# Kernel optimization log

Hardware: AMD Instinct MI355X
Metric: run time of the kernel (lower is better)

Reference implementation:

```python
import jax, jax.numpy as jnp
import numpy as np

E = 64          # num_expert
DIN = 512       # d_input
DOUT = 512      # d_output
T = 131072      # total routed tokens (sum of fwd_expert_count)


def setup_inputs() -> dict:
    key = jax.random.key(0)
    k1, k2, k3 = jax.random.split(key, 3)
    inp = jax.random.normal(k1, (T, DIN), dtype=jnp.float32)
    # FMoELinear params: weight [E, d_out, d_in], bias [E, d_out]
    weight = jax.random.normal(k2, (E, DOUT, DIN), dtype=jnp.float32) * (1.0 / np.sqrt(DIN))
    bias = jax.random.normal(k3, (E, DOUT), dtype=jnp.float32) * 0.01
    # Irregular per-expert token counts summing exactly to T (host-side int64,
    # as in fastmoe where fwd_expert_count lives on CPU and drives dispatch).
    rng = np.random.default_rng(0)
    counts = rng.multinomial(T, np.full(E, 1.0 / E))
    fwd_expert_count = np.asarray(counts, dtype=np.int64)
    return {"inp": inp, "weight": weight, "bias": bias, "fwd_expert_count": fwd_expert_count}


def reference(inp, weight, bias, fwd_expert_count):
    # Grouped GEMM: tokens are sorted by expert; expert e owns rows
    # [offs[e], offs[e+1]).  y_i = x_i @ W_e^T + b_e.
    counts = np.asarray(fwd_expert_count)
    offs = np.concatenate([[0], np.cumsum(counts)])
    outs = []
    for e in range(counts.shape[0]):  # fixed small loop over experts
        xe = inp[int(offs[e]):int(offs[e + 1])]          # [n_e, d_in]
        outs.append(xe @ weight[e].T + bias[e])          # [n_e, d_out]
    return jnp.concatenate(outs, axis=0)                 # [T, d_out]
```

## Files before the change

kernel.cpp:

```cpp
#include <hip/hip_runtime.h>
#include <hip/hip_bf16.h>
#include <stdint.h>

#define NE    64
#define DIN   512
#define DOUT  512
#define TTOK  131072
#define BM    256
#define BN    256
#define BK    32
#define NK    (DIN / BK)
#define TILES_TOTAL (TTOK / BM + NE)
#define NXCD  8
#define TPX   (TILES_TOTAL / NXCD)

typedef __bf16 bf16x8_t __attribute__((ext_vector_type(8)));
typedef float  f32x4_t  __attribute__((ext_vector_type(4)));

#define ABUF(i) ((i) * 32768)
#define BBUF(i) (65536 + (i) * 16384)
#define LDS_BYTES 98304

#define WAITV0() asm volatile("s_waitcnt vmcnt(0)" ::: "memory")
#define SB() __builtin_amdgcn_sched_barrier(0)

#define WBF_OFF 32768

__global__ void setup_tiles(const int* __restrict__ cnt, int* __restrict__ ws) {
    int e = threadIdx.x;
    if (e >= NE) return;
    int off = 0, tbase = 0;
    for (int i = 0; i < e; ++i) {
        int c = cnt[i];
        off += c;
        tbase += (c + (BM - 1)) / BM;
    }
    int c = cnt[e];
    int nt = (c + (BM - 1)) / BM;
    int* tbl = ws + 4;
    for (int t = 0; t < nt; ++t) {
        int idx = tbase + t;
        tbl[4 * idx + 0] = e;
        tbl[4 * idx + 1] = off + t * BM;
        tbl[4 * idx + 2] = off + c;
        tbl[4 * idx + 3] = 0;
    }
    if (e == NE - 1) ws[0] = tbase + nt;
}

__global__ __launch_bounds__(256) void wcvt(const float* __restrict__ w,
                                            __bf16* __restrict__ wbf) {
    const size_t stride = (size_t)gridDim.x * 256;
    size_t i = (size_t)blockIdx.x * 256 + threadIdx.x;
    const size_t n8 = (size_t)NE * DOUT * DIN / 8;
    for (; i < n8; i += stride) {
        f32x4_t a = *(const f32x4_t*)(w + i * 8);
        f32x4_t b = *(const f32x4_t*)(w + i * 8 + 4);
        bf16x8_t h;
#pragma unroll
        for (int j = 0; j < 4; ++j) {
            h[j]     = (__bf16)a[j];
            h[4 + j] = (__bf16)b[j];
        }
        *(bf16x8_t*)(wbf + i * 8) = h;
    }
}

__device__ __forceinline__ void gload16(const void* g, uint8_t* l) {
    __builtin_amdgcn_global_load_lds(
        (const __attribute__((address_space(1))) uint32_t*)g,
        (__attribute__((address_space(3))) uint32_t*)l, 16, 0, 0);
}

__global__ __launch_bounds__(1024) void moe_gemm(
    const float* __restrict__ inp,
    const __bf16* __restrict__ wbf,
    const float* __restrict__ bias,
    const int* __restrict__ ws,
    float* __restrict__ out)
{
    __shared__ __align__(16) uint8_t smem[LDS_BYTES];

    const int bid  = blockIdx.x;
    const int xcd  = bid & (NXCD - 1);
    const int slot = bid >> 3;
    const int tile = xcd * TPX + (slot >> 1);
    const int n0   = (slot & 1) * BN;

    const int ntiles = ws[0];
    if (tile >= ntiles) return;
    const int4 ti = ((const int4*)(ws + 4))[tile];
    const int e = ti.x, row0 = ti.y, row_end = ti.z;

    const int tid  = threadIdx.x;
    const int lane = tid & 63;
    const int wave = tid >> 6;
    const int dr = lane >> 3;
    const int ac = lane & 7;
    const int u  = ac ^ dr;

    const float* asrc[2];
#pragma unroll
    for (int i = 0; i < 2; ++i) {
        int arow = wave * 16 + i * 8 + dr;
        int grow = row0 + arow;
        if (grow > row_end - 1) grow = row_end - 1;
        asrc[i] = inp + (size_t)grow * DIN + (u << 2);
    }
    auto issueA = [&](int t, int buf) {
        uint8_t* dst = smem + ABUF(buf) + wave * 2048;
#pragma unroll
        for (int i = 0; i < 2; ++i)
            gload16(asrc[i] + t * BK, dst + i * 1024);
    };

    const int lr_st = wave * 8 + dr;
    const int dout  = n0 + lr_st + ((u >> 2) << 7);
    const __bf16* bsrc = wbf + (size_t)(e * DOUT + dout) * DIN + (u & 3) * 8;
    auto issueB = [&](int t, int buf) {
        gload16(bsrc + t * BK, smem + BBUF(buf) + wave * 1024);
    };

    const int wr = (wave >> 2) * 64;
    const int wc = (wave & 3) * 64;
    const int frow = lane & 15;
    const int kg   = lane >> 4;

    f32x4_t acc[4][4] = {};

    auto compute = [&](int buf) {
        bf16x8_t af[4], bg[4];
#pragma unroll
        for (int m = 0; m < 4; ++m) {
            const int row = wr + m * 16 + frow;
            const uint8_t* pa = smem + ABUF(buf) + row * 128;
            const int sw = (row & 7) << 4;
            f32x4_t q0 = *(const f32x4_t*)(pa + ((kg * 32)      ^ sw));
            f32x4_t q1 = *(const f32x4_t*)(pa + ((kg * 32 + 16) ^ sw));
#pragma unroll
            for (int j = 0; j < 4; ++j) {
                af[m][j]     = (__bf16)q0[j];
                af[m][4 + j] = (__bf16)q1[j];
            }
        }
#pragma unroll
        for (int n = 0; n < 4; ++n) {
            const int row = wc + n * 16 + frow;
            const int lr  = row & 127;
            const int h   = row >> 7;
            bg[n] = *(const bf16x8_t*)(smem + BBUF(buf) + lr * 128 +
                                       ((h * 64 + kg * 16) ^ ((lr & 7) << 4)));
        }
        __builtin_amdgcn_s_setprio(1);
#pragma unroll
        for (int m = 0; m < 4; ++m)
#pragma unroll
            for (int n = 0; n < 4; ++n)
                acc[m][n] = __builtin_amdgcn_mfma_f32_16x16x32_bf16(
                    af[m], bg[n], acc[m][n], 0, 0, 0);
        __builtin_amdgcn_s_setprio(0);
    };

    issueA(0, 0);
    issueB(0, 0);
    WAITV0(); SB();
    __builtin_amdgcn_s_barrier();
#pragma unroll
    for (int t = 0; t < NK; ++t) {
        const int buf = t & 1;
        if (t + 1 < NK) {
            issueA(t + 1, buf ^ 1);
            issueB(t + 1, buf ^ 1);
        }
        compute(buf);
        if (t + 1 < NK) {
            WAITV0(); SB();
            __builtin_amdgcn_s_barrier();
        }
    }

    const int crow = kg * 4;
    const int ccol = frow;
    float bv[4];
#pragma unroll
    for (int n = 0; n < 4; ++n)
        bv[n] = bias[e * DOUT + n0 + wc + n * 16 + ccol];
#pragma unroll
    for (int m = 0; m < 4; ++m) {
#pragma unroll
        for (int j = 0; j < 4; ++j) {
            const int grow = row0 + wr + m * 16 + crow + j;
            if (grow < row_end) {
                float* orow = out + (size_t)grow * DOUT + n0 + wc + ccol;
#pragma unroll
                for (int n = 0; n < 4; ++n)
                    orow[n * 16] = acc[m][n][j] + bv[n];
            }
        }
    }
}

extern "C" void kernel_launch(void* const* d_in, const int* in_sizes, int n_in,
                              void* d_out, int out_size, void* d_ws, size_t ws_size,
                              hipStream_t stream) {
    const float* inp    = (const float*)d_in[0];
    const float* weight = (const float*)d_in[1];
    const float* bias   = (const float*)d_in[2];
    const int* cnt      = (const int*)d_in[3];
    float* out = (float*)d_out;
    int* ws = (int*)d_ws;
    __bf16* wbf = (__bf16*)((char*)d_ws + WBF_OFF);

    hipLaunchKernelGGL(setup_tiles, dim3(1), dim3(64), 0, stream, cnt, ws);
    hipLaunchKernelGGL(wcvt, dim3(2048), dim3(256), 0, stream, weight, wbf);
    hipLaunchKernelGGL(moe_gemm, dim3(TILES_TOTAL * 2), dim3(1024), 0, stream,
                       inp, wbf, bias, ws, out);
}
```

Before: 200.0 us.

## Halve M tile, load weight fragments directly from global, shrink blocks to 512 threads

Reduces the row tile from 256 to 128 and the block from 1024 to 512 threads (8 waves). B-operand (bf16 weight) fragments are now read straight from global memory into registers each K step, with no LDS staging, so only the A tile is double-buffered in LDS. LDS use drops from 96KB to 32KB, and launch bounds of 512 with 4 blocks per CU are meant to let more blocks share a CU and hide latency. The cost is uncoalesced per-lane global weight loads that are not shared across waves, plus roughly twice as many tiles and so more redundant weight traffic.

Result: slower. 283.1 us (+41.6%).

```diff
diff --git a/kernel.cpp b/kernel.cpp
--- a/kernel.cpp
+++ b/kernel.cpp
@@ -6,7 +6,7 @@
 #define DIN   512
 #define DOUT  512
 #define TTOK  131072
-#define BM    256
+#define BM    128
 #define BN    256
 #define BK    32
 #define NK    (DIN / BK)
@@ -17,9 +17,8 @@
 typedef __bf16 bf16x8_t __attribute__((ext_vector_type(8)));
 typedef float  f32x4_t  __attribute__((ext_vector_type(4)));
 
-#define ABUF(i) ((i) * 32768)
-#define BBUF(i) (65536 + (i) * 16384)
-#define LDS_BYTES 98304
+#define ABUF(i) ((i) * 16384)
+#define LDS_BYTES 32768
 
 #define WAITV0() asm volatile("s_waitcnt vmcnt(0)" ::: "memory")
 #define SB() __builtin_amdgcn_sched_barrier(0)
@@ -72,7 +71,7 @@
         (__attribute__((address_space(3))) uint32_t*)l, 16, 0, 0);
 }
 
-__global__ __launch_bounds__(1024) void moe_gemm(
+__global__ __launch_bounds__(512, 4) void moe_gemm(
     const float* __restrict__ inp,
     const __bf16* __restrict__ wbf,
     const float* __restrict__ bias,
@@ -114,22 +113,27 @@
             gload16(asrc[i] + t * BK, dst + i * 1024);
     };
 
-    const int lr_st = wave * 8 + dr;
-    const int dout  = n0 + lr_st + ((u >> 2) << 7);
-    const __bf16* bsrc = wbf + (size_t)(e * DOUT + dout) * DIN + (u & 3) * 8;
-    auto issueB = [&](int t, int buf) {
-        gload16(bsrc + t * BK, smem + BBUF(buf) + wave * 1024);
-    };
-
     const int wr = (wave >> 2) * 64;
     const int wc = (wave & 3) * 64;
     const int frow = lane & 15;
     const int kg   = lane >> 4;
 
+    const __bf16* bfrag[4];
+#pragma unroll
+    for (int n = 0; n < 4; ++n)
+        bfrag[n] = wbf + (size_t)(e * DOUT + n0 + wc + n * 16 + frow) * DIN + kg * 8;
+
     f32x4_t acc[4][4] = {};
 
+    bf16x8_t bg[4];
+    auto loadB = [&](int t) {
+#pragma unroll
+        for (int n = 0; n < 4; ++n)
+            bg[n] = *(const bf16x8_t*)(bfrag[n] + t * BK);
+    };
+
     auto compute = [&](int buf) {
-        bf16x8_t af[4], bg[4];
+        bf16x8_t af[4];
 #pragma unroll
         for (int m = 0; m < 4; ++m) {
             const int row = wr + m * 16 + frow;
@@ -143,14 +147,6 @@
                 af[m][4 + j] = (__bf16)q1[j];
             }
         }
-#pragma unroll
-        for (int n = 0; n < 4; ++n) {
-            const int row = wc + n * 16 + frow;
-            const int lr  = row & 127;
-            const int h   = row >> 7;
-            bg[n] = *(const bf16x8_t*)(smem + BBUF(buf) + lr * 128 +
-                                       ((h * 64 + kg * 16) ^ ((lr & 7) << 4)));
-        }
         __builtin_amdgcn_s_setprio(1);
 #pragma unroll
         for (int m = 0; m < 4; ++m)
@@ -162,16 +158,15 @@
     };
 
     issueA(0, 0);
-    issueB(0, 0);
     WAITV0(); SB();
     __builtin_amdgcn_s_barrier();
 #pragma unroll
     for (int t = 0; t < NK; ++t) {
         const int buf = t & 1;
-        if (t + 1 < NK) {
-            issueA(t + 1, buf ^ 1);
-            issueB(t + 1, buf ^ 1);
-        }
+        loadB(t);
+        SB();
+        if (t + 1 < NK) issueA(t + 1, buf ^ 1);
+        SB();
         compute(buf);
         if (t + 1 < NK) {
             WAITV0(); SB();
@@ -213,6 +208,6 @@
 
     hipLaunchKernelGGL(setup_tiles, dim3(1), dim3(64), 0, stream, cnt, ws);
     hipLaunchKernelGGL(wcvt, dim3(2048), dim3(256), 0, stream, weight, wbf);
-    hipLaunchKernelGGL(moe_gemm, dim3(TILES_TOTAL * 2), dim3(1024), 0, stream,
+    hipLaunchKernelGGL(moe_gemm, dim3(TILES_TOTAL * 2), dim3(512), 0, stream,
                        inp, wbf, bias, ws, out);
 }
```

## Halve M tile and stage A via registers with bf16 conversion before LDS

Applied to the files above, without the earlier changes.

The M tile shrinks to 128 and blocks drop to 512 threads with launch bounds allowing 4 blocks per CU. A is now loaded into registers as fp32, converted to bf16 once, and written to LDS in swizzled form. The compute loop then reads bf16 fragments directly instead of converting per wave. This halves LDS use and removes redundant conversions, which should raise occupancy, but the register-staged A path adds VGPR pressure and a load-to-store dependency inside the loop.

After: 205.8 us. +2.9%, slower.

```diff
diff --git a/kernel.cpp b/kernel.cpp
--- a/kernel.cpp
+++ b/kernel.cpp
@@ -6,7 +6,7 @@
 #define DIN   512
 #define DOUT  512
 #define TTOK  131072
-#define BM    256
+#define BM    128
 #define BN    256
 #define BK    32
 #define NK    (DIN / BK)
@@ -17,11 +17,12 @@
 typedef __bf16 bf16x8_t __attribute__((ext_vector_type(8)));
 typedef float  f32x4_t  __attribute__((ext_vector_type(4)));
 
-#define ABUF(i) ((i) * 32768)
-#define BBUF(i) (65536 + (i) * 16384)
-#define LDS_BYTES 98304
+#define ABUF(i) ((i) * 8192)
+#define BBUF(i) (16384 + (i) * 16384)
+#define LDS_BYTES 49152
 
 #define WAITV0() asm volatile("s_waitcnt vmcnt(0)" ::: "memory")
+#define LGKM0()  asm volatile("s_waitcnt lgkmcnt(0)" ::: "memory")
 #define SB() __builtin_amdgcn_sched_barrier(0)
 
 #define WBF_OFF 32768
@@ -72,7 +73,7 @@
         (__attribute__((address_space(3))) uint32_t*)l, 16, 0, 0);
 }
 
-__global__ __launch_bounds__(1024) void moe_gemm(
+__global__ __launch_bounds__(512, 4) void moe_gemm(
     const float* __restrict__ inp,
     const __bf16* __restrict__ wbf,
     const float* __restrict__ bias,
@@ -99,26 +100,40 @@
     const int ac = lane & 7;
     const int u  = ac ^ dr;
 
-    const float* asrc[2];
+    const __bf16* bsrc[2];
 #pragma unroll
     for (int i = 0; i < 2; ++i) {
-        int arow = wave * 16 + i * 8 + dr;
-        int grow = row0 + arow;
-        if (grow > row_end - 1) grow = row_end - 1;
-        asrc[i] = inp + (size_t)grow * DIN + (u << 2);
-    }
-    auto issueA = [&](int t, int buf) {
-        uint8_t* dst = smem + ABUF(buf) + wave * 2048;
+        int lr = wave * 16 + i * 8 + dr;
+        int dout = n0 + lr + ((u >> 2) << 7);
+        bsrc[i] = wbf + (size_t)(e * DOUT + dout) * DIN + (u & 3) * 8;
+    }
+    auto issueB = [&](int t, int buf) {
+        uint8_t* dst = smem + BBUF(buf) + wave * 2048;
 #pragma unroll
         for (int i = 0; i < 2; ++i)
-            gload16(asrc[i] + t * BK, dst + i * 1024);
-    };
-
-    const int lr_st = wave * 8 + dr;
-    const int dout  = n0 + lr_st + ((u >> 2) << 7);
-    const __bf16* bsrc = wbf + (size_t)(e * DOUT + dout) * DIN + (u & 3) * 8;
-    auto issueB = [&](int t, int buf) {
-        gload16(bsrc + t * BK, smem + BBUF(buf) + wave * 1024);
+            gload16(bsrc[i] + t * BK, dst + i * 1024);
+    };
+
+    const int alr = tid >> 3;
+    const int acn = tid & 7;
+    int agrow = row0 + alr + ((acn >> 2) << 6);
+    if (agrow > row_end - 1) agrow = row_end - 1;
+    const float* asrc = inp + (size_t)agrow * DIN + (acn & 3) * 8;
+    const int awoff = alr * 128 + ((acn * 16) ^ ((alr & 7) << 4));
+
+    f32x4_t ra[2];
+    auto loadA = [&](int t) {
+        ra[0] = *(const f32x4_t*)(asrc + t * BK);
+        ra[1] = *(const f32x4_t*)(asrc + t * BK + 4);
+    };
+    auto writeA = [&](int buf) {
+        bf16x8_t h;
+#pragma unroll
+        for (int j = 0; j < 4; ++j) {
+            h[j]     = (__bf16)ra[0][j];
+            h[4 + j] = (__bf16)ra[1][j];
+        }
+        *(bf16x8_t*)(smem + ABUF(buf) + awoff) = h;
     };
 
     const int wr = (wave >> 2) * 64;
@@ -133,15 +148,10 @@
 #pragma unroll
         for (int m = 0; m < 4; ++m) {
             const int row = wr + m * 16 + frow;
-            const uint8_t* pa = smem + ABUF(buf) + row * 128;
-            const int sw = (row & 7) << 4;
-            f32x4_t q0 = *(const f32x4_t*)(pa + ((kg * 32)      ^ sw));
-            f32x4_t q1 = *(const f32x4_t*)(pa + ((kg * 32 + 16) ^ sw));
-#pragma unroll
-            for (int j = 0; j < 4; ++j) {
-                af[m][j]     = (__bf16)q0[j];
-                af[m][4 + j] = (__bf16)q1[j];
-            }
+            const int lr  = row & 63;
+            const int h   = row >> 6;
+            af[m] = *(const bf16x8_t*)(smem + ABUF(buf) + lr * 128 +
+                                       ((h * 64 + kg * 16) ^ ((lr & 7) << 4)));
         }
 #pragma unroll
         for (int n = 0; n < 4; ++n) {
@@ -161,20 +171,24 @@
         __builtin_amdgcn_s_setprio(0);
     };
 
-    issueA(0, 0);
+    loadA(0);
     issueB(0, 0);
-    WAITV0(); SB();
+    writeA(0);
+    WAITV0(); LGKM0(); SB();
     __builtin_amdgcn_s_barrier();
 #pragma unroll
     for (int t = 0; t < NK; ++t) {
         const int buf = t & 1;
         if (t + 1 < NK) {
-            issueA(t + 1, buf ^ 1);
+            loadA(t + 1);
+            SB();
             issueB(t + 1, buf ^ 1);
+            SB();
         }
         compute(buf);
         if (t + 1 < NK) {
-            WAITV0(); SB();
+            writeA(buf ^ 1);
+            WAITV0(); LGKM0(); SB();
             __builtin_amdgcn_s_barrier();
         }
     }
@@ -213,6 +227,6 @@
 
     hipLaunchKernelGGL(setup_tiles, dim3(1), dim3(64), 0, stream, cnt, ws);
     hipLaunchKernelGGL(wcvt, dim3(2048), dim3(256), 0, stream, weight, wbf);
-    hipLaunchKernelGGL(moe_gemm, dim3(TILES_TOTAL * 2), dim3(1024), 0, stream,
+    hipLaunchKernelGGL(moe_gemm, dim3(TILES_TOTAL * 2), dim3(512), 0, stream,
                        inp, wbf, bias, ws, out);
 }
```

## Convert A to bf16 once in registers and pipeline a BK=64 loop with 512 threads

Applied to the files above, without the earlier changes.

The A tile is now loaded from global memory into registers, converted to bf16 and written to swizzled LDS once per tile. Previously fp32 was staged in LDS and every wave reconverted it on each read. BK doubles to 64, blocks shrink to 512 threads, each wave computes a 128x64 output, and the loop is split into four LDS-read/MFMA phases with interleaved global prefetch and barriers. This reduces LDS footprint per element and conversion work, but adds more barriers, more register pressure from 32 accumulators, and 128KB of LDS that limits the block to one per CU despite the launch bound of 2.

Result: faster. 192.8 us (-3.6%).

```diff
diff --git a/kernel.cpp b/kernel.cpp
--- a/kernel.cpp
+++ b/kernel.cpp
@@ -8,8 +8,8 @@
 #define TTOK  131072
 #define BM    256
 #define BN    256
-#define BK    32
-#define NK    (DIN / BK)
+#define BK    64
+#define NKT   (DIN / BK)
 #define TILES_TOTAL (TTOK / BM + NE)
 #define NXCD  8
 #define TPX   (TILES_TOTAL / NXCD)
@@ -18,11 +18,13 @@
 typedef float  f32x4_t  __attribute__((ext_vector_type(4)));
 
 #define ABUF(i) ((i) * 32768)
-#define BBUF(i) (65536 + (i) * 16384)
-#define LDS_BYTES 98304
-
-#define WAITV0() asm volatile("s_waitcnt vmcnt(0)" ::: "memory")
+#define BBUF(i) (65536 + (i) * 32768)
+#define LDS_BYTES 131072
+
+#define WAITV(n) asm volatile("s_waitcnt vmcnt(" #n ")" ::: "memory")
+#define LGKM0()  asm volatile("s_waitcnt lgkmcnt(0)" ::: "memory")
 #define SB() __builtin_amdgcn_sched_barrier(0)
+#define BAR() __builtin_amdgcn_s_barrier()
 
 #define WBF_OFF 32768
 
@@ -72,7 +74,7 @@
         (__attribute__((address_space(3))) uint32_t*)l, 16, 0, 0);
 }
 
-__global__ __launch_bounds__(1024) void moe_gemm(
+__global__ __launch_bounds__(512, 2) void moe_gemm(
     const float* __restrict__ inp,
     const __bf16* __restrict__ wbf,
     const float* __restrict__ bias,
@@ -95,88 +97,138 @@
     const int tid  = threadIdx.x;
     const int lane = tid & 63;
     const int wave = tid >> 6;
+
+    const int arow = tid >> 3;
+    const int acn  = tid & 7;
+    const int aswz = (arow & 7) << 4;
+    const float* asrc[4];
+    int awoff[4];
+#pragma unroll
+    for (int i = 0; i < 4; ++i) {
+        int r = arow + 64 * i;
+        int grow = row0 + r;
+        if (grow > row_end - 1) grow = row_end - 1;
+        asrc[i]  = inp + (size_t)grow * DIN + acn * 8;
+        awoff[i] = r * 128 + ((acn * 16) ^ aswz);
+    }
+    f32x4_t ra[8];
+    auto issueAglb = [&](int tk) {
+#pragma unroll
+        for (int i = 0; i < 4; ++i) {
+            ra[2 * i]     = *(const f32x4_t*)(asrc[i] + tk * BK);
+            ra[2 * i + 1] = *(const f32x4_t*)(asrc[i] + tk * BK + 4);
+        }
+    };
+    auto cvtWriteA = [&](int buf) {
+#pragma unroll
+        for (int i = 0; i < 4; ++i) {
+            bf16x8_t h;
+#pragma unroll
+            for (int j = 0; j < 4; ++j) {
+                h[j]     = (__bf16)ra[2 * i][j];
+                h[4 + j] = (__bf16)ra[2 * i + 1][j];
+            }
+            *(bf16x8_t*)(smem + ABUF(buf) + awoff[i]) = h;
+        }
+    };
+
     const int dr = lane >> 3;
     const int ac = lane & 7;
     const int u  = ac ^ dr;
-
-    const float* asrc[2];
-#pragma unroll
-    for (int i = 0; i < 2; ++i) {
-        int arow = wave * 16 + i * 8 + dr;
-        int grow = row0 + arow;
-        if (grow > row_end - 1) grow = row_end - 1;
-        asrc[i] = inp + (size_t)grow * DIN + (u << 2);
-    }
-    auto issueA = [&](int t, int buf) {
-        uint8_t* dst = smem + ABUF(buf) + wave * 2048;
-#pragma unroll
-        for (int i = 0; i < 2; ++i)
-            gload16(asrc[i] + t * BK, dst + i * 1024);
-    };
-
-    const int lr_st = wave * 8 + dr;
-    const int dout  = n0 + lr_st + ((u >> 2) << 7);
-    const __bf16* bsrc = wbf + (size_t)(e * DOUT + dout) * DIN + (u & 3) * 8;
-    auto issueB = [&](int t, int buf) {
-        gload16(bsrc + t * BK, smem + BBUF(buf) + wave * 1024);
-    };
-
-    const int wr = (wave >> 2) * 64;
+    const __bf16* bsrc[4];
+#pragma unroll
+    for (int i = 0; i < 4; ++i) {
+        int row = wave * 32 + i * 8 + dr;
+        bsrc[i] = wbf + (size_t)(e * DOUT + n0 + row) * DIN + u * 8;
+    }
+    auto issueB = [&](int tk, int buf) {
+        uint8_t* dst = smem + BBUF(buf) + wave * 4096;
+#pragma unroll
+        for (int i = 0; i < 4; ++i)
+            gload16(bsrc[i] + tk * BK, dst + i * 1024);
+    };
+
+    const int wr = (wave >> 2) * 128;
     const int wc = (wave & 3) * 64;
     const int frow = lane & 15;
     const int kg   = lane >> 4;
 
-    f32x4_t acc[4][4] = {};
-
-    auto compute = [&](int buf) {
-        bf16x8_t af[4], bg[4];
-#pragma unroll
-        for (int m = 0; m < 4; ++m) {
-            const int row = wr + m * 16 + frow;
-            const uint8_t* pa = smem + ABUF(buf) + row * 128;
-            const int sw = (row & 7) << 4;
-            f32x4_t q0 = *(const f32x4_t*)(pa + ((kg * 32)      ^ sw));
-            f32x4_t q1 = *(const f32x4_t*)(pa + ((kg * 32 + 16) ^ sw));
-#pragma unroll
-            for (int j = 0; j < 4; ++j) {
-                af[m][j]     = (__bf16)q0[j];
-                af[m][4 + j] = (__bf16)q1[j];
-            }
-        }
+    f32x4_t acc[8][4] = {};
+    bf16x8_t bg[4][2], af[2][2];
+
+    auto dsrB = [&](int buf) {
 #pragma unroll
         for (int n = 0; n < 4; ++n) {
             const int row = wc + n * 16 + frow;
-            const int lr  = row & 127;
-            const int h   = row >> 7;
-            bg[n] = *(const bf16x8_t*)(smem + BBUF(buf) + lr * 128 +
-                                       ((h * 64 + kg * 16) ^ ((lr & 7) << 4)));
-        }
+            const uint8_t* p = smem + BBUF(buf) + row * 128;
+            const int sw = (row & 7) << 4;
+#pragma unroll
+            for (int ks = 0; ks < 2; ++ks)
+                bg[n][ks] = *(const bf16x8_t*)(p + ((ks * 64 + kg * 16) ^ sw));
+        }
+    };
+    auto dsrA = [&](int buf, int q) {
+#pragma unroll
+        for (int j = 0; j < 2; ++j) {
+            const int row = wr + (2 * q + j) * 16 + frow;
+            const uint8_t* p = smem + ABUF(buf) + row * 128;
+            const int sw = (row & 7) << 4;
+#pragma unroll
+            for (int ks = 0; ks < 2; ++ks)
+                af[j][ks] = *(const bf16x8_t*)(p + ((ks * 64 + kg * 16) ^ sw));
+        }
+    };
+    auto mfmaQ = [&](int q) {
         __builtin_amdgcn_s_setprio(1);
 #pragma unroll
-        for (int m = 0; m < 4; ++m)
-#pragma unroll
-            for (int n = 0; n < 4; ++n)
-                acc[m][n] = __builtin_amdgcn_mfma_f32_16x16x32_bf16(
-                    af[m], bg[n], acc[m][n], 0, 0, 0);
+        for (int ks = 0; ks < 2; ++ks)
+#pragma unroll
+            for (int j = 0; j < 2; ++j)
+#pragma unroll
+                for (int n = 0; n < 4; ++n)
+                    acc[2 * q + j][n] = __builtin_amdgcn_mfma_f32_16x16x32_bf16(
+                        af[j][ks], bg[n][ks], acc[2 * q + j][n], 0, 0, 0);
         __builtin_amdgcn_s_setprio(0);
     };
 
-    issueA(0, 0);
+    issueAglb(0);
     issueB(0, 0);
-    WAITV0(); SB();
-    __builtin_amdgcn_s_barrier();
-#pragma unroll
-    for (int t = 0; t < NK; ++t) {
+    WAITV(4); SB();
+    cvtWriteA(0);
+    issueAglb(1);
+    WAITV(8); LGKM0(); SB();
+    BAR();
+
+#pragma unroll
+    for (int t = 0; t < NKT; ++t) {
         const int buf = t & 1;
-        if (t + 1 < NK) {
-            issueA(t + 1, buf ^ 1);
-            issueB(t + 1, buf ^ 1);
-        }
-        compute(buf);
-        if (t + 1 < NK) {
-            WAITV0(); SB();
-            __builtin_amdgcn_s_barrier();
-        }
+        if (t + 1 < NKT) {
+            WAITV(0); SB();
+            cvtWriteA(buf ^ 1);
+            issueB(t + 1, buf ^ 1); SB();
+        }
+        dsrB(buf);
+        dsrA(buf, 0); SB();
+        BAR(); LGKM0(); SB();
+        mfmaQ(0);
+        BAR();
+        if (t + 2 < NKT) { issueAglb(t + 2); SB(); }
+        dsrA(buf, 1); SB();
+        BAR(); LGKM0(); SB();
+        mfmaQ(1);
+        BAR();
+        dsrA(buf, 2); SB();
+        BAR(); LGKM0(); SB();
+        mfmaQ(2);
+        BAR();
+        dsrA(buf, 3);
+        if (t + 1 < NKT) {
+            if (t + 2 < NKT) { WAITV(8); } else { WAITV(0); }
+        }
+        SB();
+        BAR(); LGKM0(); SB();
+        mfmaQ(3);
+        BAR();
     }
 
     const int crow = kg * 4;
@@ -186,7 +238,7 @@
     for (int n = 0; n < 4; ++n)
         bv[n] = bias[e * DOUT + n0 + wc + n * 16 + ccol];
 #pragma unroll
-    for (int m = 0; m < 4; ++m) {
+    for (int m = 0; m < 8; ++m) {
 #pragma unroll
         for (int j = 0; j < 4; ++j) {
             const int grow = row0 + wr + m * 16 + crow + j;
@@ -213,6 +265,6 @@
 
     hipLaunchKernelGGL(setup_tiles, dim3(1), dim3(64), 0, stream, cnt, ws);
     hipLaunchKernelGGL(wcvt, dim3(2048), dim3(256), 0, stream, weight, wbf);
-    hipLaunchKernelGGL(moe_gemm, dim3(TILES_TOTAL * 2), dim3(1024), 0, stream,
+    hipLaunchKernelGGL(moe_gemm, dim3(TILES_TOTAL * 2), dim3(512), 0, stream,
                        inp, wbf, bias, ws, out);
 }
```
